# Kernel optimization log

Hardware: AMD Instinct MI355X
Metric: run time of the kernel (lower is better)

## Reference

```python
import jax, jax.numpy as jnp
import numpy as np

N = 32768
E = 262144
OUT = 512
H = 8
DH = OUT // H


def setup_inputs() -> dict:
    key = jax.random.key(0)
    ks = jax.random.split(key, 12)
    s = 0.02
    return {
        "h": jax.random.normal(ks[0], (N, 512), dtype=jnp.float32),
        "row": jax.random.randint(ks[1], (E,), 0, N, dtype=jnp.int32),
        "col": jax.random.randint(ks[2], (E,), 0, N, dtype=jnp.int32),
        "W_in": jax.random.normal(ks[3], (512, OUT), dtype=jnp.float32) * s,
        "b_in": jnp.zeros((OUT,), dtype=jnp.float32),
        "W_q": jax.random.normal(ks[4], (OUT, OUT), dtype=jnp.float32) * s,
        "b_q": jnp.zeros((OUT,), dtype=jnp.float32),
        "W_k": jax.random.normal(ks[5], (OUT, OUT), dtype=jnp.float32) * s,
        "b_k": jnp.zeros((OUT,), dtype=jnp.float32),
        "W_v": jax.random.normal(ks[6], (OUT, OUT), dtype=jnp.float32) * s,
        "b_v": jnp.zeros((OUT,), dtype=jnp.float32),
    }


def reference(h, row, col, W_in, b_in, W_q, b_q, W_k, b_k, W_v, b_v):
    scaling = DH ** -0.5
    x = h @ W_in + b_in                                   # [N, OUT]
    q = ((x @ W_q + b_q) * scaling).reshape(N, H, DH)     # [N, H, DH]
    k = (x @ W_k + b_k).reshape(N, H, DH)
    v = (x @ W_v + b_v).reshape(N, H, DH)

    # bsddmm: per-edge, per-head attention logits only at adjacency nonzeros
    logits = jnp.einsum("ehd,ehd->eh", q[row], k[col])    # [E, H]

    # sparse row-wise softmax over each node's incident edges
    m = jax.ops.segment_max(logits, row, num_segments=N)  # [N, H]
    ex = jnp.exp(logits - m[row])                         # [E, H]
    denom = jax.ops.segment_sum(ex, row, num_segments=N)  # [N, H]
    attn = ex / denom[row]                                # [E, H]

    # bspmm: aggregate v over neighbors with sparse attention weights
    out = jax.ops.segment_sum(attn[:, :, None] * v[col], row, num_segments=N)  # [N, H, DH]
    return out
```

## Files before the change

kernel.cpp:

```cpp
#include <hip/hip_runtime.h>

#define NN 32768
#define EE 262144
#define DM 512
#define NQKV 1536
#define NHEAD 8
#define DHEAD 64

typedef unsigned short u16;
typedef unsigned int u32;
typedef __attribute__((ext_vector_type(8))) short bf16x8;
typedef __attribute__((ext_vector_type(4))) float f32x4;
typedef __attribute__((ext_vector_type(8))) u16 u16x8;
typedef __attribute__((ext_vector_type(4))) u32 u32x4;

__device__ __forceinline__ float bf2f(u16 u) {
  union { u32 i; float f; } x; x.i = ((u32)u) << 16; return x.f;
}
__device__ __forceinline__ float bflo(u32 p) {
  union { u32 i; float f; } x; x.i = p << 16; return x.f;
}
__device__ __forceinline__ float bfhi(u32 p) {
  union { u32 i; float f; } x; x.i = p & 0xFFFF0000u; return x.f;
}
__device__ __forceinline__ u16 f2bf(float f) {
  union { float f; u32 i; } x; x.f = f;
  u32 r = x.i + 0x7FFFu + ((x.i >> 16) & 1u);
  return (u16)(r >> 16);
}

__device__ __forceinline__ void load_lds16(const u16* g, u16* l) {
  __builtin_amdgcn_global_load_lds(
      (const __attribute__((address_space(1))) char*)(const void*)g,
      (__attribute__((address_space(3))) char*)(void*)l, 16, 0, 0);
}

__device__ __forceinline__ int swz(int r, int s) {
  return s ^ (r & 3) ^ ((r >> 2) & 1);
}


__global__ void tcast_w(const float* __restrict__ Wq, const float* __restrict__ Wk,
                        const float* __restrict__ Wv, u16* __restrict__ At) {
  const int z = blockIdx.z;
  const float* W = (z == 0) ? Wq : (z == 1) ? Wk : Wv;
  const float scale = (z == 0) ? 0.125f : 1.0f;
  const int m0 = blockIdx.x * 64;
  const int j0 = blockIdx.y * 64;
  __shared__ float t[64][65];
  const int tx = threadIdx.x & 63, ty = threadIdx.x >> 6;
#pragma unroll
  for (int i = 0; i < 16; ++i) {
    const int r = ty * 16 + i;
    t[r][tx] = W[(size_t)(m0 + r) * 512 + (j0 + tx)];
  }
  __syncthreads();
#pragma unroll
  for (int i = 0; i < 16; ++i) {
    const int j = j0 + ty * 16 + i;
    const int pr = (z == 0) ? j : (512 + 2 * j + (z - 1));
    At[(size_t)pr * 512 + (m0 + tx)] = f2bf(t[tx][ty * 16 + i] * scale);
  }
}

__global__ void cast_win(const float* __restrict__ Win, u16* __restrict__ Winb) {
  const int i = (blockIdx.x * 256 + threadIdx.x) * 8;
  float4 a = *(const float4*)&Win[i];
  float4 b = *(const float4*)&Win[i + 4];
  u16x8 o = { f2bf(a.x), f2bf(a.y), f2bf(a.z), f2bf(a.w),
              f2bf(b.x), f2bf(b.y), f2bf(b.z), f2bf(b.w) };
  *(u16x8*)&Winb[i] = o;
}

__global__ void make_bias(const float* __restrict__ bin,
                          const float* __restrict__ Wq, const float* __restrict__ bq,
                          const float* __restrict__ Wk, const float* __restrict__ bk,
                          const float* __restrict__ Wv, const float* __restrict__ bv,
                          float* __restrict__ bias) {
  const int j = blockIdx.x * 256 + threadIdx.x;
  if (j >= 1536) return;
  const float* Wsel; const float* bsel; int jj; float scale = 1.0f; int pos;
  if (j < 512)       { Wsel = Wq; bsel = bq; jj = j;        scale = 0.125f; pos = j; }
  else if (j < 1024) { Wsel = Wk; bsel = bk; jj = j - 512;  pos = 512 + 2 * jj; }
  else               { Wsel = Wv; bsel = bv; jj = j - 1024; pos = 513 + 2 * jj; }
  float s = 0.f;
  for (int m = 0; m < 512; ++m) s = fmaf(bin[m], Wsel[m * 512 + jj], s);
  bias[pos] = (s + bsel[jj]) * scale;
}

__global__ void cast_h(const float* __restrict__ h, u16* __restrict__ hb) {
  const int i = (blockIdx.x * 256 + threadIdx.x) * 8;
  float4 a = *(const float4*)&h[i];
  float4 b = *(const float4*)&h[i + 4];
  u16x8 o = { f2bf(a.x), f2bf(a.y), f2bf(a.z), f2bf(a.w),
              f2bf(b.x), f2bf(b.y), f2bf(b.z), f2bf(b.w) };
  *(u16x8*)&hb[i] = o;
}

__global__ void count_deg(const int* __restrict__ row, int* __restrict__ deg) {
  const int e = blockIdx.x * 256 + threadIdx.x;
  atomicAdd(&deg[row[e]], 1);
}

__global__ void scan_deg(const int* __restrict__ deg, int* __restrict__ row_ptr,
                         int* __restrict__ cursor) {
  __shared__ int sums[1024];
  const int t = threadIdx.x;
  const int base = t * 32;
  int loc[32];
  int s = 0;
#pragma unroll
  for (int i = 0; i < 32; ++i) { loc[i] = s; s += deg[base + i]; }
  sums[t] = s;
  __syncthreads();
  for (int off = 1; off < 1024; off <<= 1) {
    int v = (t >= off) ? sums[t - off] : 0;
    __syncthreads();
    sums[t] += v;
    __syncthreads();
  }
  const int excl = sums[t] - s;
#pragma unroll
  for (int i = 0; i < 32; ++i) {
    const int val = excl + loc[i];
    row_ptr[base + i] = val;
    cursor[base + i] = val;
  }
  if (t == 1023) row_ptr[NN] = sums[1023];
}

__global__ void fill_csr(const int* __restrict__ row, const int* __restrict__ col,
                         int* __restrict__ cursor, int* __restrict__ dst) {
  const int e = blockIdx.x * 256 + threadIdx.x;
  const int r = row[e];
  const int p = atomicAdd(&cursor[r], 1);
  dst[p] = col[e];
}

__global__ __launch_bounds__(256, 2) void gemm_wt(
    const u16* __restrict__ A,
    const u16* __restrict__ B,
    u16* __restrict__ C) {
  __shared__ u16 As[128 * 32];
  __shared__ u16 Bs[128 * 32];
  const int tid = threadIdx.x;
  const int lane = tid & 63;
  const int wave = tid >> 6;
  const int quad = lane >> 4;
  const int l16 = lane & 15;
  const int m0 = blockIdx.y * 128;
  const int n0 = blockIdx.x * 128;
  const int wm = (wave >> 1) * 64;
  const int wn = (wave & 1) * 64;

  const int c0 = tid, c1 = tid + 256;
  const int r0 = c0 >> 2, ko0 = swz(r0, c0 & 3) * 8;
  const int r1 = c1 >> 2, ko1 = swz(r1, c1 & 3) * 8;
  const u16* Ag0 = A + (size_t)(m0 + r0) * DM + ko0;
  const u16* Ag1 = A + (size_t)(m0 + r1) * DM + ko1;
  const u16* Bg0 = B + (size_t)(n0 + r0) * DM + ko0;
  const u16* Bg1 = B + (size_t)(n0 + r1) * DM + ko1;
  u16* Al0 = &As[c0 * 8]; u16* Al1 = &As[c1 * 8];
  u16* Bl0 = &Bs[c0 * 8]; u16* Bl1 = &Bs[c1 * 8];

  f32x4 acc[4][4];
#pragma unroll
  for (int i = 0; i < 4; ++i)
#pragma unroll
    for (int j = 0; j < 4; ++j) acc[i][j] = (f32x4){0.f, 0.f, 0.f, 0.f};

  for (int kt = 0; kt < DM; kt += 32) {
    load_lds16(Ag0 + kt, Al0);
    load_lds16(Bg0 + kt, Bl0);
    load_lds16(Ag1 + kt, Al1);
    load_lds16(Bg1 + kt, Bl1);
    __syncthreads();
    bf16x8 a[4], b[4];
#pragma unroll
    for (int i = 0; i < 4; ++i) {
      const int ra = wm + i * 16 + l16;
      const int rb = wn + i * 16 + l16;
      a[i] = *(const bf16x8*)&As[ra * 32 + swz(ra, quad) * 8];
      b[i] = *(const bf16x8*)&Bs[rb * 32 + swz(rb, quad) * 8];
    }
#pragma unroll
    for (int mi = 0; mi < 4; ++mi)
#pragma unroll
      for (int ni = 0; ni < 4; ++ni)
        acc[mi][ni] = __builtin_amdgcn_mfma_f32_16x16x32_bf16(a[mi], b[ni], acc[mi][ni], 0, 0, 0);
    __syncthreads();
  }

#pragma unroll
  for (int ni = 0; ni < 4; ++ni) {
    const int coln = n0 + wn + ni * 16 + l16;
#pragma unroll
    for (int mi = 0; mi < 4; ++mi) {
#pragma unroll
      for (int r = 0; r < 4; ++r) {
        const int rowm = m0 + wm + mi * 16 + quad * 4 + r;
        C[(size_t)rowm * 512 + coln] = f2bf(acc[mi][ni][r]);
      }
    }
  }
}

__global__ __launch_bounds__(256, 2) void gemm_qkv(
    const u16* __restrict__ A,
    const u16* __restrict__ B,
    const float* __restrict__ bias,
    u16* __restrict__ C) {
  __shared__ u16 As[128 * 32];
  __shared__ u16 Bs[128 * 32];
  const int tid = threadIdx.x;
  const int lane = tid & 63;
  const int wave = tid >> 6;
  const int quad = lane >> 4;
  const int l16 = lane & 15;
  const int m0 = blockIdx.y * 128;
  const int n0 = blockIdx.x * 128;
  const int wm = (wave >> 1) * 64;
  const int wn = (wave & 1) * 64;

  const int c0 = tid, c1 = tid + 256;
  const int r0 = c0 >> 2, ko0 = swz(r0, c0 & 3) * 8;
  const int r1 = c1 >> 2, ko1 = swz(r1, c1 & 3) * 8;
  const u16* Ag0 = A + (size_t)(m0 + r0) * DM + ko0;
  const u16* Ag1 = A + (size_t)(m0 + r1) * DM + ko1;
  const u16* Bg0 = B + (size_t)(n0 + r0) * DM + ko0;
  const u16* Bg1 = B + (size_t)(n0 + r1) * DM + ko1;
  u16* Al0 = &As[c0 * 8]; u16* Al1 = &As[c1 * 8];
  u16* Bl0 = &Bs[c0 * 8]; u16* Bl1 = &Bs[c1 * 8];

  f32x4 acc[4][4];
#pragma unroll
  for (int i = 0; i < 4; ++i)
#pragma unroll
    for (int j = 0; j < 4; ++j) acc[i][j] = (f32x4){0.f, 0.f, 0.f, 0.f};

  for (int kt = 0; kt < DM; kt += 32) {
    load_lds16(Ag0 + kt, Al0);
    load_lds16(Bg0 + kt, Bl0);
    load_lds16(Ag1 + kt, Al1);
    load_lds16(Bg1 + kt, Bl1);
    __syncthreads();
    bf16x8 a[4], b[4];
#pragma unroll
    for (int i = 0; i < 4; ++i) {
      const int ra = wm + i * 16 + l16;
      const int rb = wn + i * 16 + l16;
      a[i] = *(const bf16x8*)&As[ra * 32 + swz(ra, quad) * 8];
      b[i] = *(const bf16x8*)&Bs[rb * 32 + swz(rb, quad) * 8];
    }
#pragma unroll
    for (int mi = 0; mi < 4; ++mi)
#pragma unroll
      for (int ni = 0; ni < 4; ++ni)
        acc[mi][ni] = __builtin_amdgcn_mfma_f32_16x16x32_bf16(a[mi], b[ni], acc[mi][ni], 0, 0, 0);
    __syncthreads();
  }

#pragma unroll
  for (int ni = 0; ni < 4; ++ni) {
    const int coln = n0 + wn + ni * 16 + l16;
    const float bv = bias[coln];
#pragma unroll
    for (int mi = 0; mi < 4; ++mi) {
#pragma unroll
      for (int r = 0; r < 4; ++r) {
        const int rowm = m0 + wm + mi * 16 + quad * 4 + r;
        C[(size_t)rowm * NQKV + coln] = f2bf(acc[mi][ni][r] + bv);
      }
    }
  }
}

__global__ __launch_bounds__(256) void attn_agg(
    const u16* __restrict__ qkv16, const u32* __restrict__ qkv32,
    const int* __restrict__ row_ptr, const int* __restrict__ dst,
    float* __restrict__ out) {
  const int gt = blockIdx.x * 256 + threadIdx.x;
  const int node = gt >> 6;
  const int lane = gt & 63;
  const u16x8 qr = *(const u16x8*)&qkv16[(size_t)node * NQKV + lane * 8];
  float qf[8];
#pragma unroll
  for (int j = 0; j < 8; ++j) qf[j] = bf2f(qr[j]);

  const int beg = row_ptr[node];
  const int end = row_ptr[node + 1];
  float acc[8] = {0.f,0.f,0.f,0.f,0.f,0.f,0.f,0.f};
  float denom = 0.f;

  for (int e = beg; e < end; e += 4) {
    u32 p[4][8];
    int idx[4];
#pragma unroll
    for (int jj = 0; jj < 4; ++jj) {
      const int ee = min(e + jj, end - 1);
      idx[jj] = dst[ee];
    }
#pragma unroll
    for (int jj = 0; jj < 4; ++jj) {
      const u32* pp = qkv32 + (size_t)idx[jj] * 768 + 256 + lane * 8;
      *(u32x4*)&p[jj][0] = *(const u32x4*)pp;
      *(u32x4*)&p[jj][4] = *(const u32x4*)(pp + 4);
    }
#pragma unroll
    for (int jj = 0; jj < 4; ++jj) {
      float s = 0.f;
#pragma unroll
      for (int j = 0; j < 8; ++j) s = fmaf(qf[j], bflo(p[jj][j]), s);
      s += __shfl_xor(s, 1, 64);
      s += __shfl_xor(s, 2, 64);
      s += __shfl_xor(s, 4, 64);
      const float ex = (e + jj < end) ? __expf(s) : 0.f;
      denom += ex;
#pragma unroll
      for (int j = 0; j < 8; ++j) acc[j] = fmaf(ex, bfhi(p[jj][j]), acc[j]);
    }
  }

  const float inv = (end > beg) ? (1.0f / denom) : 0.f;
  float4 o0 = { acc[0] * inv, acc[1] * inv, acc[2] * inv, acc[3] * inv };
  float4 o1 = { acc[4] * inv, acc[5] * inv, acc[6] * inv, acc[7] * inv };
  float* op = &out[(size_t)node * 512 + lane * 8];
  *(float4*)op = o0;
  *(float4*)(op + 4) = o1;
}

extern "C" void kernel_launch(void* const* d_in, const int* in_sizes, int n_in,
                              void* d_out, int out_size, void* d_ws, size_t ws_size,
                              hipStream_t stream) {
  const float* h   = (const float*)d_in[0];
  const int*   row = (const int*)d_in[1];
  const int*   col = (const int*)d_in[2];
  const float* Win = (const float*)d_in[3];
  const float* bin = (const float*)d_in[4];
  const float* Wq  = (const float*)d_in[5];
  const float* bq  = (const float*)d_in[6];
  const float* Wk  = (const float*)d_in[7];
  const float* bk  = (const float*)d_in[8];
  const float* Wv  = (const float*)d_in[9];
  const float* bv  = (const float*)d_in[10];
  float* out = (float*)d_out;

  char* ws = (char*)d_ws;
  u16*   qkv     = (u16*)(ws + 0);
  u16*   hb      = (u16*)(ws + 100663296);
  u16*   Wt      = (u16*)(ws + 134217728);
  float* bias    = (float*)(ws + 135790592);
  int*   deg     = (int*)(ws + 135796736);
  int*   row_ptr = (int*)(ws + 135927808);
  int*   cursor  = (int*)(ws + 136058888);
  int*   dst     = (int*)(ws + 136189960);
  u16*   At      = (u16*)(ws + 0);
  u16*   Winb    = (u16*)(ws + 1572864);

  (void)hipMemsetAsync(deg, 0, NN * sizeof(int), stream);
  hipLaunchKernelGGL(tcast_w,   dim3(8, 8, 3), dim3(256), 0, stream, Wq, Wk, Wv, At);
  hipLaunchKernelGGL(cast_win,  dim3((512 * 512 / 8) / 256), dim3(256), 0, stream, Win, Winb);
  hipLaunchKernelGGL(make_bias, dim3(6), dim3(256), 0, stream, bin, Wq, bq, Wk, bk, Wv, bv, bias);
  hipLaunchKernelGGL(cast_h,    dim3((NN * DM / 8) / 256), dim3(256), 0, stream, h, hb);
  hipLaunchKernelGGL(count_deg, dim3(EE / 256), dim3(256), 0, stream, row, deg);
  hipLaunchKernelGGL(scan_deg,  dim3(1), dim3(1024), 0, stream, deg, row_ptr, cursor);
  hipLaunchKernelGGL(fill_csr,  dim3(EE / 256), dim3(256), 0, stream, row, col, cursor, dst);
  hipLaunchKernelGGL(gemm_wt,   dim3(512 / 128, 1536 / 128), dim3(256), 0, stream, At, Winb, Wt);
  hipLaunchKernelGGL(gemm_qkv,  dim3(NQKV / 128, NN / 128), dim3(256), 0, stream, hb, Wt, bias, qkv);
  hipLaunchKernelGGL(attn_agg,  dim3((NN * 64) / 256), dim3(256), 0, stream,
                     qkv, (const u32*)qkv, row_ptr, dst, out);
}
```

Baseline: 380.9 us.

## Double-buffer LDS tiles in GEMMs and swizzle QKV block order

Both bf16 GEMM kernels now use two LDS buffers, so the global-to-LDS load of the next K tile is issued before the MFMAs on the current tile, and one barrier per iteration is dropped. The goal is to hide global load latency behind compute. The QKV GEMM also remaps block indices so that blocks in the same group of eight share tiles, aiming for better L2 reuse. LDS use per block doubles to 32 KB, which could limit occupancy, and the fully unrolled K loop increases register pressure.

```diff
diff --git a/kernel.cpp b/kernel.cpp
--- a/kernel.cpp
+++ b/kernel.cpp
@@ -141,8 +141,8 @@
     const u16* __restrict__ A,
     const u16* __restrict__ B,
     u16* __restrict__ C) {
-  __shared__ u16 As[128 * 32];
-  __shared__ u16 Bs[128 * 32];
+  __shared__ u16 As[2][128 * 32];
+  __shared__ u16 Bs[2][128 * 32];
   const int tid = threadIdx.x;
   const int lane = tid & 63;
   const int wave = tid >> 6;
@@ -160,8 +160,6 @@
   const u16* Ag1 = A + (size_t)(m0 + r1) * DM + ko1;
   const u16* Bg0 = B + (size_t)(n0 + r0) * DM + ko0;
   const u16* Bg1 = B + (size_t)(n0 + r1) * DM + ko1;
-  u16* Al0 = &As[c0 * 8]; u16* Al1 = &As[c1 * 8];
-  u16* Bl0 = &Bs[c0 * 8]; u16* Bl1 = &Bs[c1 * 8];
 
   f32x4 acc[4][4];
 #pragma unroll
@@ -169,19 +167,26 @@
 #pragma unroll
     for (int j = 0; j < 4; ++j) acc[i][j] = (f32x4){0.f, 0.f, 0.f, 0.f};
 
-  for (int kt = 0; kt < DM; kt += 32) {
-    load_lds16(Ag0 + kt, Al0);
-    load_lds16(Bg0 + kt, Bl0);
-    load_lds16(Ag1 + kt, Al1);
-    load_lds16(Bg1 + kt, Bl1);
-    __syncthreads();
+  load_lds16(Ag0, &As[0][c0 * 8]);
+  load_lds16(Bg0, &Bs[0][c0 * 8]);
+  load_lds16(Ag1, &As[0][c1 * 8]);
+  load_lds16(Bg1, &Bs[0][c1 * 8]);
+  __syncthreads();
+
+  int cur = 0;
+#pragma unroll
+  for (int kt = 32; kt < DM; kt += 32) {
+    load_lds16(Ag0 + kt, &As[cur ^ 1][c0 * 8]);
+    load_lds16(Bg0 + kt, &Bs[cur ^ 1][c0 * 8]);
+    load_lds16(Ag1 + kt, &As[cur ^ 1][c1 * 8]);
+    load_lds16(Bg1 + kt, &Bs[cur ^ 1][c1 * 8]);
     bf16x8 a[4], b[4];
 #pragma unroll
     for (int i = 0; i < 4; ++i) {
       const int ra = wm + i * 16 + l16;
       const int rb = wn + i * 16 + l16;
-      a[i] = *(const bf16x8*)&As[ra * 32 + swz(ra, quad) * 8];
-      b[i] = *(const bf16x8*)&Bs[rb * 32 + swz(rb, quad) * 8];
+      a[i] = *(const bf16x8*)&As[cur][ra * 32 + swz(ra, quad) * 8];
+      b[i] = *(const bf16x8*)&Bs[cur][rb * 32 + swz(rb, quad) * 8];
     }
 #pragma unroll
     for (int mi = 0; mi < 4; ++mi)
@@ -189,6 +194,22 @@
       for (int ni = 0; ni < 4; ++ni)
         acc[mi][ni] = __builtin_amdgcn_mfma_f32_16x16x32_bf16(a[mi], b[ni], acc[mi][ni], 0, 0, 0);
     __syncthreads();
+    cur ^= 1;
+  }
+  {
+    bf16x8 a[4], b[4];
+#pragma unroll
+    for (int i = 0; i < 4; ++i) {
+      const int ra = wm + i * 16 + l16;
+      const int rb = wn + i * 16 + l16;
+      a[i] = *(const bf16x8*)&As[cur][ra * 32 + swz(ra, quad) * 8];
+      b[i] = *(const bf16x8*)&Bs[cur][rb * 32 + swz(rb, quad) * 8];
+    }
+#pragma unroll
+    for (int mi = 0; mi < 4; ++mi)
+#pragma unroll
+      for (int ni = 0; ni < 4; ++ni)
+        acc[mi][ni] = __builtin_amdgcn_mfma_f32_16x16x32_bf16(a[mi], b[ni], acc[mi][ni], 0, 0, 0);
   }
 
 #pragma unroll
@@ -210,15 +231,20 @@
     const u16* __restrict__ B,
     const float* __restrict__ bias,
     u16* __restrict__ C) {
-  __shared__ u16 As[128 * 32];
-  __shared__ u16 Bs[128 * 32];
+  __shared__ u16 As[2][128 * 32];
+  __shared__ u16 Bs[2][128 * 32];
   const int tid = threadIdx.x;
   const int lane = tid & 63;
   const int wave = tid >> 6;
   const int quad = lane >> 4;
   const int l16 = lane & 15;
-  const int m0 = blockIdx.y * 128;
-  const int n0 = blockIdx.x * 128;
+
+  const int bid = blockIdx.y * 12 + blockIdx.x;
+  const int sw = (bid & 7) * 384 + (bid >> 3);
+  const int bx = sw % 12;
+  const int by = sw / 12;
+  const int m0 = by * 128;
+  const int n0 = bx * 128;
   const int wm = (wave >> 1) * 64;
   const int wn = (wave & 1) * 64;
 
@@ -229,8 +255,6 @@
   const u16* Ag1 = A + (size_t)(m0 + r1) * DM + ko1;
   const u16* Bg0 = B + (size_t)(n0 + r0) * DM + ko0;
   const u16* Bg1 = B + (size_t)(n0 + r1) * DM + ko1;
-  u16* Al0 = &As[c0 * 8]; u16* Al1 = &As[c1 * 8];
-  u16* Bl0 = &Bs[c0 * 8]; u16* Bl1 = &Bs[c1 * 8];
 
   f32x4 acc[4][4];
 #pragma unroll
@@ -238,19 +262,26 @@
 #pragma unroll
     for (int j = 0; j < 4; ++j) acc[i][j] = (f32x4){0.f, 0.f, 0.f, 0.f};
 
-  for (int kt = 0; kt < DM; kt += 32) {
-    load_lds16(Ag0 + kt, Al0);
-    load_lds16(Bg0 + kt, Bl0);
-    load_lds16(Ag1 + kt, Al1);
-    load_lds16(Bg1 + kt, Bl1);
-    __syncthreads();
+  load_lds16(Ag0, &As[0][c0 * 8]);
+  load_lds16(Bg0, &Bs[0][c0 * 8]);
+  load_lds16(Ag1, &As[0][c1 * 8]);
+  load_lds16(Bg1, &Bs[0][c1 * 8]);
+  __syncthreads();
+
+  int cur = 0;
+#pragma unroll
+  for (int kt = 32; kt < DM; kt += 32) {
+    load_lds16(Ag0 + kt, &As[cur ^ 1][c0 * 8]);
+    load_lds16(Bg0 + kt, &Bs[cur ^ 1][c0 * 8]);
+    load_lds16(Ag1 + kt, &As[cur ^ 1][c1 * 8]);
+    load_lds16(Bg1 + kt, &Bs[cur ^ 1][c1 * 8]);
     bf16x8 a[4], b[4];
 #pragma unroll
     for (int i = 0; i < 4; ++i) {
       const int ra = wm + i * 16 + l16;
       const int rb = wn + i * 16 + l16;
-      a[i] = *(const bf16x8*)&As[ra * 32 + swz(ra, quad) * 8];
-      b[i] = *(const bf16x8*)&Bs[rb * 32 + swz(rb, quad) * 8];
+      a[i] = *(const bf16x8*)&As[cur][ra * 32 + swz(ra, quad) * 8];
+      b[i] = *(const bf16x8*)&Bs[cur][rb * 32 + swz(rb, quad) * 8];
     }
 #pragma unroll
     for (int mi = 0; mi < 4; ++mi)
@@ -258,6 +289,22 @@
       for (int ni = 0; ni < 4; ++ni)
         acc[mi][ni] = __builtin_amdgcn_mfma_f32_16x16x32_bf16(a[mi], b[ni], acc[mi][ni], 0, 0, 0);
     __syncthreads();
+    cur ^= 1;
+  }
+  {
+    bf16x8 a[4], b[4];
+#pragma unroll
+    for (int i = 0; i < 4; ++i) {
+      const int ra = wm + i * 16 + l16;
+      const int rb = wn + i * 16 + l16;
+      a[i] = *(const bf16x8*)&As[cur][ra * 32 + swz(ra, quad) * 8];
+      b[i] = *(const bf16x8*)&Bs[cur][rb * 32 + swz(rb, quad) * 8];
+    }
+#pragma unroll
+    for (int mi = 0; mi < 4; ++mi)
+#pragma unroll
+      for (int ni = 0; ni < 4; ++ni)
+        acc[mi][ni] = __builtin_amdgcn_mfma_f32_16x16x32_bf16(a[mi], b[ni], acc[mi][ni], 0, 0, 0);
   }
 
 #pragma unroll
```

Measured after the change: 370.4 us. 2.7% less time.
